# Kernel optimization log

Hardware: AMD Instinct MI355X
Metric: run time of the kernel (lower is better)

## Reference

```python
import jax, jax.numpy as jnp
import numpy as np

HIDDEN = 768
HEADS = 12
HEAD_DIM = HIDDEN // HEADS


def setup_inputs() -> dict:
    key = jax.random.key(0)
    ks = jax.random.split(key, 6)
    B, N = 32, 577  # N = 1 CLS + 576 patches
    x = jax.random.normal(ks[0], (B, N, HIDDEN), dtype=jnp.float32)
    seg_bias = jax.random.uniform(ks[1], (B, N - 1), dtype=jnp.float32)
    w_qkv = jax.random.normal(ks[2], (HIDDEN, 3 * HIDDEN), dtype=jnp.float32) * 0.02
    b_qkv = jnp.zeros((3 * HIDDEN,), dtype=jnp.float32)
    w_proj = jax.random.normal(ks[3], (HIDDEN, HIDDEN), dtype=jnp.float32) * 0.02
    b_proj = jnp.zeros((HIDDEN,), dtype=jnp.float32)
    seg_scale = jnp.ones((), dtype=jnp.float32)
    return {"x": x, "seg_bias": seg_bias, "w_qkv": w_qkv, "b_qkv": b_qkv,
            "w_proj": w_proj, "b_proj": b_proj, "seg_scale": seg_scale}


def reference(x, seg_bias, w_qkv, b_qkv, w_proj, b_proj, seg_scale):
    B, N, _ = x.shape
    scale = HEAD_DIM ** -0.5
    qkv = x @ w_qkv + b_qkv                       # (B, N, 3*H*D)
    qkv = qkv.reshape(B, N, 3, HEADS, HEAD_DIM)
    q = qkv[:, :, 0].transpose(0, 2, 1, 3)        # (B, H, N, D)
    k = qkv[:, :, 1].transpose(0, 2, 1, 3)
    v = qkv[:, :, 2].transpose(0, 2, 1, 3)
    attn = jnp.einsum('bhqd,bhkd->bhqk', q, k) * scale  # (B, H, N, N)
    # additive seg bias on CLS-query row, patch keys only (cols 1:)
    bias = (seg_bias * seg_scale)[:, None, None, :]     # (B,1,1,N-1)
    attn = attn.at[:, :, 0:1, 1:].add(bias)
    attn = jax.nn.softmax(attn, axis=-1)
    out = jnp.einsum('bhqk,bhkd->bhqd', attn, v)        # (B, H, N, D)
    out = out.transpose(0, 2, 1, 3).reshape(B, N, HIDDEN)
    return out @ w_proj + b_proj
```

## Files before the change

kernel.cpp:

```cpp
#include <hip/hip_runtime.h>


typedef unsigned short bf16_t;
typedef __attribute__((ext_vector_type(8))) short short8;
typedef __attribute__((ext_vector_type(4))) short short4v;
typedef __attribute__((ext_vector_type(4))) float f32x4;

#define B_    32
#define N_    577
#define BN_   18464
#define HID_  768
#define NH_   12
#define HD_   64
#define QKVC_ 2304
#define NPAD_ 640
#define PB_LD 68

#define CAST_BLKS 13848
#define TQKV_BLKS (72 * 24)
#define TPRJ_BLKS (24 * 24)

__device__ __forceinline__ bf16_t f2bf(float f) {
  union { float f; unsigned u; } x; x.f = f;
  unsigned r = x.u + 0x7fffu + ((x.u >> 16) & 1u);
  return (bf16_t)(r >> 16);
}

__device__ __forceinline__ unsigned cvt_pk_bf16(float a, float b) {
  unsigned r;
  asm("v_cvt_pk_bf16_f32 %0, %1, %2" : "=v"(r) : "v"(a), "v"(b));
  return r;
}

__device__ __forceinline__ void transpose_tile(const float* __restrict__ in,
                                               bf16_t* __restrict__ out,
                                               int C, int bx, int by, int tid) {
  __shared__ float tile[32][33];
  const int R = HID_;
  int c0 = bx * 32, r0 = by * 32;
  int tx = tid & 31, ty = tid >> 5;
  #pragma unroll
  for (int i = ty; i < 32; i += 8)
    tile[i][tx] = in[(size_t)(r0 + i) * C + c0 + tx];
  __syncthreads();
  #pragma unroll
  for (int i = ty; i < 32; i += 8)
    out[(size_t)(c0 + i) * R + r0 + tx] = f2bf(tile[tx][i]);
}

__global__ __launch_bounds__(256) void prep_kernel(
    const float* __restrict__ x, bf16_t* __restrict__ xb,
    const float* __restrict__ w_qkv, bf16_t* __restrict__ wqkvT,
    const float* __restrict__ w_proj, bf16_t* __restrict__ wprojT) {
  const int bid = blockIdx.x;
  const int tid = threadIdx.x;
  if (bid < CAST_BLKS) {
    int i = bid * 256 + tid;
    float4 v = ((const float4*)x)[i];
    ushort4 o;
    o.x = f2bf(v.x); o.y = f2bf(v.y); o.z = f2bf(v.z); o.w = f2bf(v.w);
    ((ushort4*)xb)[i] = o;
  } else if (bid < CAST_BLKS + TQKV_BLKS) {
    int t = bid - CAST_BLKS;
    transpose_tile(w_qkv, wqkvT, QKVC_, t % 72, t / 72, tid);
  } else {
    int t = bid - CAST_BLKS - TQKV_BLKS;
    transpose_tile(w_proj, wprojT, HID_, t % 24, t / 24, tid);
  }
}

template <int OUT_BF16>
__global__ __launch_bounds__(256, 3) void gemm_bf16_kernel(
    const bf16_t* __restrict__ A,
    const bf16_t* __restrict__ Bt,
    const float* __restrict__ bias,
    void* __restrict__ Cout,
    int M, int Nc) {
  __shared__ bf16_t As[128 * 64];
  __shared__ bf16_t Bs[128 * 64];

  const int tid  = threadIdx.x;
  const int lane = tid & 63, w = tid >> 6;
  const int quad = lane >> 4, l16 = lane & 15;

  const int Mb = (M + 127) >> 7;
  const int Nb = Nc >> 7;
  const int np_full = Mb >> 3;
  const int rem = Mb - np_full * 8;
  int bid = blockIdx.x;
  int m_blk, n_blk;
  int body = np_full * 8 * Nb;
  if (bid < body) {
    int p = bid / (8 * Nb), local = bid % (8 * Nb);
    m_blk = p * 8 + (local & 7);
    n_blk = local >> 3;
  } else {
    int t = bid - body;
    m_blk = np_full * 8 + t % rem;
    n_blk = t / rem;
  }
  const int m0 = m_blk * 128, n0 = n_blk * 128;
  const int wm = (w >> 1) * 64, wn = (w & 1) * 64;
  const bool mfull = (m0 + 128 <= M);

  f32x4 acc[4][4];
  #pragma unroll
  for (int i = 0; i < 4; ++i)
    #pragma unroll
    for (int j = 0; j < 4; ++j)
      acc[i][j] = (f32x4){0.f, 0.f, 0.f, 0.f};

  for (int kt = 0; kt < 768; kt += 64) {
    __syncthreads();
    if (mfull) {
      #pragma unroll
      for (int it = 0; it < 4; ++it) {
        int gi = it * 256 + tid;
        int row = gi >> 3, chp = gi & 7;
        int ch = chp ^ (row & 7);
        __builtin_amdgcn_global_load_lds(
            (const __attribute__((address_space(1))) unsigned int*)(A + (size_t)(m0 + row) * 768 + kt + ch * 8),
            (__attribute__((address_space(3))) unsigned int*)(As + gi * 8),
            16, 0, 0);
        __builtin_amdgcn_global_load_lds(
            (const __attribute__((address_space(1))) unsigned int*)(Bt + (size_t)(n0 + row) * 768 + kt + ch * 8),
            (__attribute__((address_space(3))) unsigned int*)(Bs + gi * 8),
            16, 0, 0);
      }
    } else {
      #pragma unroll
      for (int it = 0; it < 4; ++it) {
        int gi = it * 256 + tid;
        int row = gi >> 3, chp = gi & 7;
        int ch = chp ^ (row & 7);
        int gm = m0 + row; if (gm >= M) gm = M - 1;
        __builtin_amdgcn_global_load_lds(
            (const __attribute__((address_space(1))) unsigned int*)(A + (size_t)gm * 768 + kt + ch * 8),
            (__attribute__((address_space(3))) unsigned int*)(As + gi * 8),
            16, 0, 0);
        __builtin_amdgcn_global_load_lds(
            (const __attribute__((address_space(1))) unsigned int*)(Bt + (size_t)(n0 + row) * 768 + kt + ch * 8),
            (__attribute__((address_space(3))) unsigned int*)(Bs + gi * 8),
            16, 0, 0);
      }
    }
    __syncthreads();

    #pragma unroll
    for (int ks = 0; ks < 2; ++ks) {
      short8 af[4], bfr[4];
      #pragma unroll
      for (int i = 0; i < 4; ++i) {
        int row = wm + i * 16 + l16;
        int c = ks * 4 + quad;
        af[i] = *(const short8*)(As + row * 64 + (c ^ (row & 7)) * 8);
      }
      #pragma unroll
      for (int j = 0; j < 4; ++j) {
        int row = wn + j * 16 + l16;
        int c = ks * 4 + quad;
        bfr[j] = *(const short8*)(Bs + row * 64 + (c ^ (row & 7)) * 8);
      }
      #pragma unroll
      for (int i = 0; i < 4; ++i)
        #pragma unroll
        for (int j = 0; j < 4; ++j)
          acc[i][j] = __builtin_amdgcn_mfma_f32_16x16x32_bf16(af[i], bfr[j], acc[i][j], 0, 0, 0);
    }
  }

  #pragma unroll
  for (int i = 0; i < 4; ++i) {
    int mrow_base = m0 + wm + i * 16 + quad * 4;
    #pragma unroll
    for (int j = 0; j < 4; ++j) {
      int col = n0 + wn + j * 16 + l16;
      float bs = bias[col];
      #pragma unroll
      for (int r = 0; r < 4; ++r) {
        int row = mrow_base + r;
        if (row < M) {
          float v = acc[i][j][r] + bs;
          if (OUT_BF16)
            ((bf16_t*)Cout)[(size_t)row * Nc + col] = f2bf(v);
          else
            ((float*)Cout)[(size_t)row * Nc + col] = v;
        }
      }
    }
  }
}

__global__ __launch_bounds__(256) void vt_kernel(const bf16_t* __restrict__ qkv,
                                                 bf16_t* __restrict__ vT) {
  const int t = blockIdx.x, h = blockIdx.y, b = blockIdx.z;
  const int tid = threadIdx.x;
  __shared__ bf16_t Ls[64 * 65];
  const int kv0 = t * 64;
  const bf16_t* Vp = qkv + (size_t)b * N_ * QKVC_ + 2 * HID_ + h * HD_;

  #pragma unroll
  for (int it = 0; it < 2; ++it) {
    int idx = it * 256 + tid;
    int row = idx >> 3, ch = idx & 7;
    int krow = kv0 + row; if (krow > N_ - 1) krow = N_ - 1;
    short8 v8 = *(const short8*)(Vp + (size_t)krow * QKVC_ + ch * 8);
    #pragma unroll
    for (int j = 0; j < 8; ++j)
      Ls[(ch * 8 + j) * 65 + row] = (bf16_t)v8[j];
  }
  __syncthreads();
  bf16_t* outp = vT + ((size_t)(b * NH_ + h) * HD_) * NPAD_;
  #pragma unroll
  for (int it = 0; it < 2; ++it) {
    int idx = it * 256 + tid;
    int d = idx >> 3, kc = idx & 7;
    short8 o8;
    #pragma unroll
    for (int j = 0; j < 8; ++j) {
      int p = kc * 8 + j;
      int ky = ((p & 3) << 4) | (p >> 2);
      o8[j] = (short)Ls[d * 65 + ky];
    }
    *(short8*)(outp + (size_t)d * NPAD_ + kv0 + kc * 8) = o8;
  }
}

template <int MI>
__device__ __forceinline__ void attn_body(
    int b, int h, int qbase,
    const bf16_t* __restrict__ qkv, const bf16_t* __restrict__ vT,
    const float* __restrict__ seg_bias, const float* __restrict__ seg_scale,
    bf16_t* __restrict__ out,
    bf16_t* Ks0, bf16_t* Ks1, bf16_t* Vt0, bf16_t* Vt1, bf16_t* PbAll) {
  const int tid = threadIdx.x;
  const int w = tid >> 6, lane = tid & 63;
  const int quad = lane >> 4, l16 = lane & 15;
  const int xsw = l16 & 7;

  const bf16_t* Qbase = qkv + (size_t)b * N_ * QKVC_ + h * HD_;
  const bf16_t* Kbase = Qbase + HID_;
  const bf16_t* Vtb   = vT + ((size_t)(b * NH_ + h) * HD_) * NPAD_;

  const float ssl = seg_scale[0] * 1.44269504f;

  {
    int row = tid >> 3;
    int ch = (tid & 7) ^ (row & 7);
    __builtin_amdgcn_global_load_lds(
        (const __attribute__((address_space(1))) unsigned int*)(Kbase + (size_t)row * QKVC_ + ch * 8),
        (__attribute__((address_space(3))) unsigned int*)(Ks0 + tid * 8), 16, 0, 0);
    __builtin_amdgcn_global_load_lds(
        (const __attribute__((address_space(1))) unsigned int*)(Vtb + (size_t)row * NPAD_ + ch * 8),
        (__attribute__((address_space(3))) unsigned int*)(Vt0 + tid * 8), 16, 0, 0);
  }

  const int q0 = qbase + w * (MI * 16);
  short8 qf[MI][2];
  #pragma unroll
  for (int mi = 0; mi < MI; ++mi) {
    int qr = q0 + mi * 16 + l16;
    if (qr > N_ - 1) qr = N_ - 1;
    qf[mi][0] = *(const short8*)(Qbase + (size_t)qr * QKVC_ + quad * 8);
    qf[mi][1] = *(const short8*)(Qbase + (size_t)qr * QKVC_ + 32 + quad * 8);
  }
  const float qsc = 0.125f * 1.44269504f;
  #pragma unroll
  for (int mi = 0; mi < MI; ++mi)
    #pragma unroll
    for (int c = 0; c < 2; ++c)
      #pragma unroll
      for (int j = 0; j < 8; ++j) {
        unsigned u = ((unsigned)(unsigned short)qf[mi][c][j]) << 16;
        union { unsigned u; float f; } x; x.u = u;
        qf[mi][c][j] = (short)f2bf(x.f * qsc);
      }

  const f32x4 z4 = {0.f, 0.f, 0.f, 0.f};
  f32x4 o[MI][4];
  f32x4 ls[MI];
  #pragma unroll
  for (int mi = 0; mi < MI; ++mi) {
    ls[mi] = z4;
    #pragma unroll
    for (int j = 0; j < 4; ++j) o[mi][j] = z4;
  }

  short8 ones;
  #pragma unroll
  for (int j = 0; j < 8; ++j) ones[j] = (short)0x3F80;

  const bool bias_wave = (qbase == 0 && w == 0);
  bf16_t* pw = PbAll + w * 16 * PB_LD;

  for (int t = 0; t < 9; ++t) {
    const int cur = t & 1;

    __builtin_amdgcn_s_barrier();
    __builtin_amdgcn_sched_barrier(0);

    {
      const int kv1 = (t + 1) * 64;
      bf16_t* ksn = cur ? Ks0 : Ks1;
      bf16_t* vtn = cur ? Vt0 : Vt1;
      int row = tid >> 3;
      int ch = (tid & 7) ^ (row & 7);
      int krow = kv1 + row; if (krow > N_ - 1) krow = N_ - 1;
      __builtin_amdgcn_global_load_lds(
          (const __attribute__((address_space(1))) unsigned int*)(Kbase + (size_t)krow * QKVC_ + ch * 8),
          (__attribute__((address_space(3))) unsigned int*)(ksn + tid * 8), 16, 0, 0);
      __builtin_amdgcn_global_load_lds(
          (const __attribute__((address_space(1))) unsigned int*)(Vtb + (size_t)row * NPAD_ + kv1 + ch * 8),
          (__attribute__((address_space(3))) unsigned int*)(vtn + tid * 8), 16, 0, 0);
    }

    asm volatile("s_waitcnt vmcnt(2)" ::: "memory");
    __builtin_amdgcn_sched_barrier(0);
    __builtin_amdgcn_s_barrier();
    __builtin_amdgcn_sched_barrier(0);

    const bf16_t* ks = cur ? Ks1 : Ks0;
    const bf16_t* vt = cur ? Vt1 : Vt0;

    f32x4 s[MI][4];
    __builtin_amdgcn_s_setprio(1);
    #pragma unroll
    for (int sub = 0; sub < 4; ++sub) {
      short8 k0 = *(const short8*)(ks + (sub * 16 + l16) * 64 + (quad ^ xsw) * 8);
      short8 k1 = *(const short8*)(ks + (sub * 16 + l16) * 64 + ((4 + quad) ^ xsw) * 8);
      #pragma unroll
      for (int mi = 0; mi < MI; ++mi) {
        s[mi][sub] = __builtin_amdgcn_mfma_f32_16x16x32_bf16(qf[mi][0], k0, z4, 0, 0, 0);
        s[mi][sub] = __builtin_amdgcn_mfma_f32_16x16x32_bf16(qf[mi][1], k1, s[mi][sub], 0, 0, 0);
      }
    }
    __builtin_amdgcn_s_setprio(0);

    if (bias_wave && quad == 0) {
      const int kv0 = t * 64;
      #pragma unroll
      for (int sub = 0; sub < 4; ++sub) {
        int key = kv0 + sub * 16 + l16;
        if (key >= 1)
          s[0][sub][0] += seg_bias[b * (N_ - 1) + key - 1] * ssl;
      }
    }

    #pragma unroll
    for (int mi = 0; mi < MI; ++mi) {
      #pragma unroll
      for (int r = 0; r < 4; ++r) {
        float p0 = __builtin_amdgcn_exp2f(s[mi][0][r]);
        float p1 = __builtin_amdgcn_exp2f(s[mi][1][r]);
        float p2 = __builtin_amdgcn_exp2f(s[mi][2][r]);
        float p3 = __builtin_amdgcn_exp2f(s[mi][3][r]);
        uint2 pk;
        pk.x = cvt_pk_bf16(p0, p1);
        pk.y = cvt_pk_bf16(p2, p3);
        *(uint2*)(pw + (quad * 4 + r) * PB_LD + l16 * 4) = pk;
      }

      const bf16_t* pr = pw + l16 * PB_LD + quad * 8;
      union { short8 v; short4v hv[2]; } pa0, pa1;
      pa0.hv[0] = *(const short4v*)(pr);
      pa0.hv[1] = *(const short4v*)(pr + 4);
      pa1.hv[0] = *(const short4v*)(pr + 32);
      pa1.hv[1] = *(const short4v*)(pr + 36);
      __builtin_amdgcn_s_setprio(1);
      ls[mi] = __builtin_amdgcn_mfma_f32_16x16x32_bf16(pa0.v, ones, ls[mi], 0, 0, 0);
      ls[mi] = __builtin_amdgcn_mfma_f32_16x16x32_bf16(pa1.v, ones, ls[mi], 0, 0, 0);
      #pragma unroll
      for (int ds = 0; ds < 4; ++ds) {
        short8 vb0 = *(const short8*)(vt + (ds * 16 + l16) * 64 + (quad ^ xsw) * 8);
        short8 vb1 = *(const short8*)(vt + (ds * 16 + l16) * 64 + ((4 + quad) ^ xsw) * 8);
        o[mi][ds] = __builtin_amdgcn_mfma_f32_16x16x32_bf16(pa0.v, vb0, o[mi][ds], 0, 0, 0);
        o[mi][ds] = __builtin_amdgcn_mfma_f32_16x16x32_bf16(pa1.v, vb1, o[mi][ds], 0, 0, 0);
      }
      __builtin_amdgcn_s_setprio(0);
    }
  }

  {
    asm volatile("s_waitcnt vmcnt(0)" ::: "memory");
    __builtin_amdgcn_sched_barrier(0);
    __builtin_amdgcn_s_barrier();
    __builtin_amdgcn_sched_barrier(0);

    const bf16_t* ks = Ks1;
    const bf16_t* vt = Vt1;

    short8 k0 = *(const short8*)(ks + l16 * 64 + (quad ^ xsw) * 8);
    short8 k1 = *(const short8*)(ks + l16 * 64 + ((4 + quad) ^ xsw) * 8);
    f32x4 s9[MI];
    #pragma unroll
    for (int mi = 0; mi < MI; ++mi) {
      s9[mi] = __builtin_amdgcn_mfma_f32_16x16x32_bf16(qf[mi][0], k0, z4, 0, 0, 0);
      s9[mi] = __builtin_amdgcn_mfma_f32_16x16x32_bf16(qf[mi][1], k1, s9[mi], 0, 0, 0);
    }
    if (bias_wave && quad == 0 && l16 == 0)
      s9[0][0] += seg_bias[b * (N_ - 1) + (N_ - 2)] * ssl;

    #pragma unroll
    for (int mi = 0; mi < MI; ++mi) {
      #pragma unroll
      for (int r = 0; r < 4; ++r) {
        float p0 = (l16 == 0) ? __builtin_amdgcn_exp2f(s9[mi][r]) : 0.f;
        uint2 pk;
        pk.x = cvt_pk_bf16(p0, 0.f);
        pk.y = 0u;
        *(uint2*)(pw + (quad * 4 + r) * PB_LD + l16 * 4) = pk;
      }
      const bf16_t* pr = pw + l16 * PB_LD + quad * 8;
      union { short8 v; short4v hv[2]; } pa0;
      pa0.hv[0] = *(const short4v*)(pr);
      pa0.hv[1] = *(const short4v*)(pr + 4);
      ls[mi] = __builtin_amdgcn_mfma_f32_16x16x32_bf16(pa0.v, ones, ls[mi], 0, 0, 0);
      #pragma unroll
      for (int ds = 0; ds < 4; ++ds) {
        short8 vb0 = *(const short8*)(vt + (ds * 16 + l16) * 64 + (quad ^ xsw) * 8);
        o[mi][ds] = __builtin_amdgcn_mfma_f32_16x16x32_bf16(pa0.v, vb0, o[mi][ds], 0, 0, 0);
      }
    }
  }

  #pragma unroll
  for (int mi = 0; mi < MI; ++mi)
    #pragma unroll
    for (int r = 0; r < 4; ++r) {
      float inv = 1.0f / ls[mi][r];
      int row = q0 + mi * 16 + quad * 4 + r;
      if (row < N_) {
        size_t base = ((size_t)b * N_ + row) * HID_ + h * HD_;
        #pragma unroll
        for (int ds = 0; ds < 4; ++ds)
          out[base + ds * 16 + l16] = f2bf(o[mi][ds][r] * inv);
      }
    }
}

__global__ __launch_bounds__(512) void attn_kernel(
    const bf16_t* __restrict__ qkv,
    const bf16_t* __restrict__ vT,
    const float* __restrict__ seg_bias,
    const float* __restrict__ seg_scale,
    bf16_t* __restrict__ out) {
  __shared__ __align__(16) bf16_t Ks[2][64 * 64];
  __shared__ __align__(16) bf16_t Vt[2][64 * 64];
  __shared__ __align__(16) bf16_t Pb[8][16 * PB_LD];

  const int bid = blockIdx.x;
  if (bid < 768) {
    const int pair = bid % 384, qblk = bid / 384;
    attn_body<2>(pair / NH_, pair % NH_, qblk * 256,
                 qkv, vT, seg_bias, seg_scale, out,
                 &Ks[0][0], &Ks[1][0], &Vt[0][0], &Vt[1][0], &Pb[0][0]);
  } else {
    const int pair = bid - 768;
    attn_body<1>(pair / NH_, pair % NH_, 512,
                 qkv, vT, seg_bias, seg_scale, out,
                 &Ks[0][0], &Ks[1][0], &Vt[0][0], &Vt[1][0], &Pb[0][0]);
  }
}

extern "C" void kernel_launch(void* const* d_in, const int* in_sizes, int n_in,
                              void* d_out, int out_size, void* d_ws, size_t ws_size,
                              hipStream_t stream) {
  const float* x         = (const float*)d_in[0];
  const float* seg_bias  = (const float*)d_in[1];
  const float* w_qkv     = (const float*)d_in[2];
  const float* b_qkv     = (const float*)d_in[3];
  const float* w_proj    = (const float*)d_in[4];
  const float* b_proj    = (const float*)d_in[5];
  const float* seg_scale = (const float*)d_in[6];

  char* ws = (char*)d_ws;
  bf16_t* xb     = (bf16_t*)ws;
  bf16_t* wqkvT  = (bf16_t*)(ws + 28360704);
  bf16_t* wprojT = (bf16_t*)(ws + 31899648);
  bf16_t* qkvb   = (bf16_t*)(ws + 33079296);
  bf16_t* vT     = (bf16_t*)(ws + 118161408);
  bf16_t* attnb  = xb;

  prep_kernel<<<CAST_BLKS + TQKV_BLKS + TPRJ_BLKS, 256, 0, stream>>>(
      x, xb, w_qkv, wqkvT, w_proj, wprojT);

  gemm_bf16_kernel<1><<<145 * (QKVC_ / 128), 256, 0, stream>>>(
      xb, wqkvT, b_qkv, (void*)qkvb, BN_, QKVC_);

  vt_kernel<<<dim3(10, NH_, B_), 256, 0, stream>>>(qkvb, vT);

  attn_kernel<<<1152, 512, 0, stream>>>(qkvb, vT, seg_bias, seg_scale, attnb);

  gemm_bf16_kernel<0><<<145 * (HID_ / 128), 256, 0, stream>>>(
      attnb, wprojT, b_proj, d_out, BN_, HID_);
}
```

Before: 298.8 us.

## Use 640-thread attention blocks covering 320 queries each, dropping tail blocks

The attention kernel now runs 768 blocks of 10 waves, each covering 320 query rows with two 16-row tiles per wave. This replaces the earlier 1152 blocks, which mixed 256-row blocks with a separate single-tile tail block per (batch, head). Only the first 512 threads stage K/V tiles into LDS, and the Pb scratch grows to 10 slots. The aim is to load each K/V tile for more query rows, remove the imbalanced tail blocks and cut launch count. The cost is fewer, larger blocks and more padded query rows at the end (640 rows for 577), which may reduce occupancy.

```diff
diff --git a/kernel.cpp b/kernel.cpp
--- a/kernel.cpp
+++ b/kernel.cpp
@@ -226,17 +226,26 @@
   }
 }
 
-template <int MI>
-__device__ __forceinline__ void attn_body(
-    int b, int h, int qbase,
-    const bf16_t* __restrict__ qkv, const bf16_t* __restrict__ vT,
-    const float* __restrict__ seg_bias, const float* __restrict__ seg_scale,
-    bf16_t* __restrict__ out,
-    bf16_t* Ks0, bf16_t* Ks1, bf16_t* Vt0, bf16_t* Vt1, bf16_t* PbAll) {
+__global__ __launch_bounds__(640, 5) void attn_kernel(
+    const bf16_t* __restrict__ qkv,
+    const bf16_t* __restrict__ vT,
+    const float* __restrict__ seg_bias,
+    const float* __restrict__ seg_scale,
+    bf16_t* __restrict__ out) {
+  __shared__ __align__(16) bf16_t Ks[2][64 * 64];
+  __shared__ __align__(16) bf16_t Vt[2][64 * 64];
+  __shared__ __align__(16) bf16_t Pb[10][16 * PB_LD];
+
+  const int bid  = blockIdx.x;
+  const int pair = bid % 384;
+  const int qblk = bid / 384;
+  const int h    = pair % NH_;
+  const int b    = pair / NH_;
   const int tid = threadIdx.x;
   const int w = tid >> 6, lane = tid & 63;
   const int quad = lane >> 4, l16 = lane & 15;
   const int xsw = l16 & 7;
+  const bool stager = (tid < 512);
 
   const bf16_t* Qbase = qkv + (size_t)b * N_ * QKVC_ + h * HD_;
   const bf16_t* Kbase = Qbase + HID_;
@@ -244,21 +253,21 @@
 
   const float ssl = seg_scale[0] * 1.44269504f;
 
-  {
+  if (stager) {
     int row = tid >> 3;
     int ch = (tid & 7) ^ (row & 7);
     __builtin_amdgcn_global_load_lds(
         (const __attribute__((address_space(1))) unsigned int*)(Kbase + (size_t)row * QKVC_ + ch * 8),
-        (__attribute__((address_space(3))) unsigned int*)(Ks0 + tid * 8), 16, 0, 0);
+        (__attribute__((address_space(3))) unsigned int*)(&Ks[0][0] + tid * 8), 16, 0, 0);
     __builtin_amdgcn_global_load_lds(
         (const __attribute__((address_space(1))) unsigned int*)(Vtb + (size_t)row * NPAD_ + ch * 8),
-        (__attribute__((address_space(3))) unsigned int*)(Vt0 + tid * 8), 16, 0, 0);
-  }
-
-  const int q0 = qbase + w * (MI * 16);
-  short8 qf[MI][2];
-  #pragma unroll
-  for (int mi = 0; mi < MI; ++mi) {
+        (__attribute__((address_space(3))) unsigned int*)(&Vt[0][0] + tid * 8), 16, 0, 0);
+  }
+
+  const int q0 = qblk * 320 + w * 32;
+  short8 qf[2][2];
+  #pragma unroll
+  for (int mi = 0; mi < 2; ++mi) {
     int qr = q0 + mi * 16 + l16;
     if (qr > N_ - 1) qr = N_ - 1;
     qf[mi][0] = *(const short8*)(Qbase + (size_t)qr * QKVC_ + quad * 8);
@@ -266,7 +275,7 @@
   }
   const float qsc = 0.125f * 1.44269504f;
   #pragma unroll
-  for (int mi = 0; mi < MI; ++mi)
+  for (int mi = 0; mi < 2; ++mi)
     #pragma unroll
     for (int c = 0; c < 2; ++c)
       #pragma unroll
@@ -277,10 +286,10 @@
       }
 
   const f32x4 z4 = {0.f, 0.f, 0.f, 0.f};
-  f32x4 o[MI][4];
-  f32x4 ls[MI];
-  #pragma unroll
-  for (int mi = 0; mi < MI; ++mi) {
+  f32x4 o[2][4];
+  f32x4 ls[2];
+  #pragma unroll
+  for (int mi = 0; mi < 2; ++mi) {
     ls[mi] = z4;
     #pragma unroll
     for (int j = 0; j < 4; ++j) o[mi][j] = z4;
@@ -290,8 +299,8 @@
   #pragma unroll
   for (int j = 0; j < 8; ++j) ones[j] = (short)0x3F80;
 
-  const bool bias_wave = (qbase == 0 && w == 0);
-  bf16_t* pw = PbAll + w * 16 * PB_LD;
+  const bool bias_wave = (qblk == 0 && w == 0);
+  bf16_t* pw = Pb[w];
 
   for (int t = 0; t < 9; ++t) {
     const int cur = t & 1;
@@ -299,10 +308,10 @@
     __builtin_amdgcn_s_barrier();
     __builtin_amdgcn_sched_barrier(0);
 
-    {
+    if (stager) {
       const int kv1 = (t + 1) * 64;
-      bf16_t* ksn = cur ? Ks0 : Ks1;
-      bf16_t* vtn = cur ? Vt0 : Vt1;
+      bf16_t* ksn = cur ? &Ks[0][0] : &Ks[1][0];
+      bf16_t* vtn = cur ? &Vt[0][0] : &Vt[1][0];
       int row = tid >> 3;
       int ch = (tid & 7) ^ (row & 7);
       int krow = kv1 + row; if (krow > N_ - 1) krow = N_ - 1;
@@ -319,17 +328,17 @@
     __builtin_amdgcn_s_barrier();
     __builtin_amdgcn_sched_barrier(0);
 
-    const bf16_t* ks = cur ? Ks1 : Ks0;
-    const bf16_t* vt = cur ? Vt1 : Vt0;
-
-    f32x4 s[MI][4];
+    const bf16_t* ks = cur ? &Ks[1][0] : &Ks[0][0];
+    const bf16_t* vt = cur ? &Vt[1][0] : &Vt[0][0];
+
+    f32x4 s[2][4];
     __builtin_amdgcn_s_setprio(1);
     #pragma unroll
     for (int sub = 0; sub < 4; ++sub) {
       short8 k0 = *(const short8*)(ks + (sub * 16 + l16) * 64 + (quad ^ xsw) * 8);
       short8 k1 = *(const short8*)(ks + (sub * 16 + l16) * 64 + ((4 + quad) ^ xsw) * 8);
       #pragma unroll
-      for (int mi = 0; mi < MI; ++mi) {
+      for (int mi = 0; mi < 2; ++mi) {
         s[mi][sub] = __builtin_amdgcn_mfma_f32_16x16x32_bf16(qf[mi][0], k0, z4, 0, 0, 0);
         s[mi][sub] = __builtin_amdgcn_mfma_f32_16x16x32_bf16(qf[mi][1], k1, s[mi][sub], 0, 0, 0);
       }
@@ -347,7 +356,7 @@
     }
 
     #pragma unroll
-    for (int mi = 0; mi < MI; ++mi) {
+    for (int mi = 0; mi < 2; ++mi) {
       #pragma unroll
       for (int r = 0; r < 4; ++r) {
         float p0 = __builtin_amdgcn_exp2f(s[mi][0][r]);
@@ -386,14 +395,14 @@
     __builtin_amdgcn_s_barrier();
     __builtin_amdgcn_sched_barrier(0);
 
-    const bf16_t* ks = Ks1;
-    const bf16_t* vt = Vt1;
+    const bf16_t* ks = &Ks[1][0];
+    const bf16_t* vt = &Vt[1][0];
 
     short8 k0 = *(const short8*)(ks + l16 * 64 + (quad ^ xsw) * 8);
     short8 k1 = *(const short8*)(ks + l16 * 64 + ((4 + quad) ^ xsw) * 8);
-    f32x4 s9[MI];
-    #pragma unroll
-    for (int mi = 0; mi < MI; ++mi) {
+    f32x4 s9[2];
+    #pragma unroll
+    for (int mi = 0; mi < 2; ++mi) {
       s9[mi] = __builtin_amdgcn_mfma_f32_16x16x32_bf16(qf[mi][0], k0, z4, 0, 0, 0);
       s9[mi] = __builtin_amdgcn_mfma_f32_16x16x32_bf16(qf[mi][1], k1, s9[mi], 0, 0, 0);
     }
@@ -401,7 +410,7 @@
       s9[0][0] += seg_bias[b * (N_ - 1) + (N_ - 2)] * ssl;
 
     #pragma unroll
-    for (int mi = 0; mi < MI; ++mi) {
+    for (int mi = 0; mi < 2; ++mi) {
       #pragma unroll
       for (int r = 0; r < 4; ++r) {
         float p0 = (l16 == 0) ? __builtin_amdgcn_exp2f(s9[mi][r]) : 0.f;
@@ -424,7 +433,7 @@
   }
 
   #pragma unroll
-  for (int mi = 0; mi < MI; ++mi)
+  for (int mi = 0; mi < 2; ++mi)
     #pragma unroll
     for (int r = 0; r < 4; ++r) {
       float inv = 1.0f / ls[mi][r];
@@ -436,30 +445,6 @@
           out[base + ds * 16 + l16] = f2bf(o[mi][ds][r] * inv);
       }
     }
-}
-
-__global__ __launch_bounds__(512) void attn_kernel(
-    const bf16_t* __restrict__ qkv,
-    const bf16_t* __restrict__ vT,
-    const float* __restrict__ seg_bias,
-    const float* __restrict__ seg_scale,
-    bf16_t* __restrict__ out) {
-  __shared__ __align__(16) bf16_t Ks[2][64 * 64];
-  __shared__ __align__(16) bf16_t Vt[2][64 * 64];
-  __shared__ __align__(16) bf16_t Pb[8][16 * PB_LD];
-
-  const int bid = blockIdx.x;
-  if (bid < 768) {
-    const int pair = bid % 384, qblk = bid / 384;
-    attn_body<2>(pair / NH_, pair % NH_, qblk * 256,
-                 qkv, vT, seg_bias, seg_scale, out,
-                 &Ks[0][0], &Ks[1][0], &Vt[0][0], &Vt[1][0], &Pb[0][0]);
-  } else {
-    const int pair = bid - 768;
-    attn_body<1>(pair / NH_, pair % NH_, 512,
-                 qkv, vT, seg_bias, seg_scale, out,
-                 &Ks[0][0], &Ks[1][0], &Vt[0][0], &Vt[1][0], &Pb[0][0]);
-  }
 }
 
 extern "C" void kernel_launch(void* const* d_in, const int* in_sizes, int n_in,
@@ -489,7 +474,7 @@
 
   vt_kernel<<<dim3(10, NH_, B_), 256, 0, stream>>>(qkvb, vT);
 
-  attn_kernel<<<1152, 512, 0, stream>>>(qkvb, vT, seg_bias, seg_scale, attnb);
+  attn_kernel<<<768, 640, 0, stream>>>(qkvb, vT, seg_bias, seg_scale, attnb);
 
   gemm_bf16_kernel<0><<<145 * (HID_ / 128), 256, 0, stream>>>(
       attnb, wprojT, b_proj, d_out, BN_, HID_);
```

Result: slower. 338.7 us (+13.4%).
